# Optimization experiments

Measured on AMD Instinct MI355X. Metric: run time of the kernel, lower is better.

The kernel has to match this reference:

```python
import jax, jax.numpy as jnp
import numpy as np

N_STATE = 64
SEQ_L = 4096
BATCH, HCH = 16, 512
DT_MIN, DT_MAX = 0.001, 0.1


def _make_DPLR_HiPPO(N):
    # HiPPO-LegS matrix and its NPLR -> DPLR decomposition (annotated-s4).
    P = np.sqrt(1 + 2 * np.arange(N))
    A = P[:, None] * P[None, :]
    A = np.tril(A) - np.diag(np.arange(N))
    nhippo = -A
    p = 0.5 * np.sqrt(2 * np.arange(1, N + 1) + 1.0)
    q = 2 * p
    S = nhippo + p[:, None] * q[None, :]
    Lambda, V = np.linalg.eig(S)
    Vc = V.conj().T
    p_t = Vc @ p
    q_t = Vc @ q.conj()
    return Lambda, p_t, q_t, Vc


def _ri(z):
    return np.stack([z.real, z.imag], axis=-1).astype(np.float32)


def setup_inputs() -> dict:
    key = jax.random.key(0)
    k_u, k_ct, k_b, k_d, k_ls = jax.random.split(key, 5)
    Lambda, p, q, Vc = _make_DPLR_HiPPO(N_STATE)
    u = jax.random.normal(k_u, (BATCH, HCH, SEQ_L), dtype=jnp.float32)
    # lecun_normal params (fan_in = N)
    Ct_ri = jax.random.normal(k_ct, (1, N_STATE, 2), dtype=jnp.float32) / np.sqrt(N_STATE)
    Bp = jax.random.normal(k_b, (N_STATE, 1), dtype=jnp.float32) / np.sqrt(N_STATE)
    D = jax.random.uniform(k_d, (1,), dtype=jnp.float32)
    log_step = jax.random.uniform(
        k_ls, (1,), dtype=jnp.float32,
        minval=np.log(DT_MIN), maxval=np.log(DT_MAX))
    return {
        "u": u,
        "Lambda_ri": jnp.asarray(_ri(Lambda)),
        "p_ri": jnp.asarray(_ri(p)),
        "q_ri": jnp.asarray(_ri(q)),
        "Vc_ri": jnp.asarray(_ri(Vc)),
        "Ct_ri": Ct_ri,
        "Bp": Bp,
        "D": D,
        "log_step": log_step,
    }


def _cplx(x_ri):
    return x_ri[..., 0] + 1j * x_ri[..., 1]


def _s4_kernel(Lambda, p, q, B, Ct, step, L):
    # DPLR generating function evaluated at the L roots of unity (K_gen_DPLR
    # + conv_from_gen), vectorized over frequencies.
    Omega = jnp.exp((-2j * jnp.pi) * (jnp.arange(L) / L))          # (L,)
    g = (2.0 / step) * ((1.0 - Omega) / (1.0 + Omega))             # (L,)
    c = 2.0 / (1.0 + Omega)                                        # (L,)
    denom = g[:, None] - Lambda[None, :]                           # (L, N)
    cauchy = lambda v: (v[None, :] / denom).sum(-1)                # (L,)
    k00 = cauchy(Ct.conj() * B)
    k01 = cauchy(Ct.conj() * p)
    k10 = cauchy(q.conj() * B)
    k11 = cauchy(q.conj() * p)
    at_roots = c * (k00 - k01 * (1.0 / (1.0 + k11)) * k10)
    return jnp.fft.ifft(at_roots, L).real                          # (L,)


def reference(u, Lambda_ri, p_ri, q_ri, Vc_ri, Ct_ri, Bp, D, log_step):
    L = u.shape[-1]
    Lambda = _cplx(Lambda_ri)
    p = _cplx(p_ri)
    q = _cplx(q_ri)
    Vc = _cplx(Vc_ri)
    Ct = _cplx(Ct_ri).reshape(-1)                  # (N,)
    B = (Vc @ Bp.astype(Vc.dtype)).reshape(-1)     # (N,) complex
    step = jnp.exp(log_step)[0]
    K = _s4_kernel(Lambda, p, q, B, Ct, step, L).astype(u.dtype)   # (L,)
    # non-circular convolution via zero-padded FFT along the last axis
    n = 2 * L
    y = jnp.fft.irfft(jnp.fft.rfft(u, n=n) * jnp.fft.rfft(K, n=n), n=n)[..., :L]
    return y + D[0] * u
```

## Files before the change

kernel.cpp:

```cpp
#include <hip/hip_runtime.h>
#include <math.h>


#define SEQ_L 4096
#define M4    4096
#define NFFT  8192
#define NST   64
#define NROWS 8192
#define TWO_PI 6.28318530717958647692f

typedef float2 cf;

__device__ __forceinline__ cf cmul(cf a, cf b){ return make_float2(a.x*b.x - a.y*b.y, a.x*b.y + a.y*b.x); }
__device__ __forceinline__ cf cadd(cf a, cf b){ return make_float2(a.x+b.x, a.y+b.y); }
__device__ __forceinline__ cf csub(cf a, cf b){ return make_float2(a.x-b.x, a.y-b.y); }
__device__ __forceinline__ double2 dcmul(double2 a, double2 b) {
  return make_double2(a.x*b.x - a.y*b.y, a.x*b.y + a.y*b.x);
}

__device__ __forceinline__ int s2f(int i){ return i ^ (((i >> 6) & 1) << 3); }
__device__ __forceinline__ int s3f(int i){ return i ^ ((i >> 6) & 7) ^ (((i >> 6) & 1) << 3); }
__device__ __forceinline__ int smf(int i){ return i ^ ((i >> 6) & 7); }

template<int S>
__device__ __forceinline__ void r4(cf& a0, cf& a1, cf& a2, cf& a3){
  cf t0 = cadd(a0,a2), t1 = csub(a0,a2);
  cf t2 = cadd(a1,a3), t3 = csub(a1,a3);
  cf w = (S < 0) ? make_float2(t3.y, -t3.x) : make_float2(-t3.y, t3.x);
  a0 = cadd(t0,t2); a2 = csub(t0,t2);
  a1 = cadd(t1,w);  a3 = csub(t1,w);
}

template<int S, bool ZHI, bool LO4=false>
__device__ __forceinline__ void dft8(cf x[8]){
  const float C = 0.70710678118654752f;
  cf e0,e1,e2,e3,o0,o1,o2,o3;
  if (ZHI) {
    cf w  = (S<0)? make_float2(x[2].y,-x[2].x) : make_float2(-x[2].y,x[2].x);
    e0 = cadd(x[0],x[2]); e2 = csub(x[0],x[2]);
    e1 = cadd(x[0],w);    e3 = csub(x[0],w);
    cf w2 = (S<0)? make_float2(x[3].y,-x[3].x) : make_float2(-x[3].y,x[3].x);
    o0 = cadd(x[1],x[3]); o2 = csub(x[1],x[3]);
    o1 = cadd(x[1],w2);   o3 = csub(x[1],w2);
  } else {
    cf a0=x[0],a1=x[2],a2=x[4],a3=x[6];
    r4<S>(a0,a1,a2,a3);  e0=a0;e1=a1;e2=a2;e3=a3;
    cf b0=x[1],b1=x[3],b2=x[5],b3=x[7];
    r4<S>(b0,b1,b2,b3);  o0=b0;o1=b1;o2=b2;o3=b3;
  }
  x[0] = cadd(e0,o0); if (!LO4) x[4] = csub(e0,o0);
  cf t1 = (S<0)? make_float2(C*(o1.x+o1.y), C*(o1.y-o1.x))
               : make_float2(C*(o1.x-o1.y), C*(o1.x+o1.y));
  x[1] = cadd(e1,t1); if (!LO4) x[5] = csub(e1,t1);
  cf t2 = (S<0)? make_float2(o2.y,-o2.x) : make_float2(-o2.y,o2.x);
  x[2] = cadd(e2,t2); if (!LO4) x[6] = csub(e2,t2);
  cf t3 = (S<0)? make_float2(C*(o3.y-o3.x), -C*(o3.x+o3.y))
               : make_float2(-C*(o3.x+o3.y), C*(o3.x-o3.y));
  x[3] = cadd(e3,t3); if (!LO4) x[7] = csub(e3,t3);
}

__device__ __forceinline__ void chain8(cf x[8], float th){
  float sn, cs; __sincosf(th, &sn, &cs);
  cf w1 = make_float2(cs, sn);
  cf w2 = cmul(w1, w1);
  cf w3 = cmul(w2, w1);
  x[1] = cmul(x[1], w1); x[2] = cmul(x[2], w2); x[3] = cmul(x[3], w3);
  cf w4 = cmul(w2, w2);
  cf w5 = cmul(w3, w2);
  cf w6 = cmul(w3, w3);
  cf w7 = cmul(w4, w3);
  x[4] = cmul(x[4], w4); x[5] = cmul(x[5], w5); x[6] = cmul(x[6], w6);
  x[7] = cmul(x[7], w7);
}

__global__ __launch_bounds__(256) void k_at(
    const float* __restrict__ Lam_ri, const float* __restrict__ p_ri,
    const float* __restrict__ q_ri,  const float* __restrict__ Vc_ri,
    const float* __restrict__ Ct_ri, const float* __restrict__ Bp,
    const float* __restrict__ log_step, float2* __restrict__ atroots) {
  __shared__ double2 lam[NST], ctB[NST], ctp[NST], qB[NST], qp[NST];
  __shared__ double stepd;
  int tx = threadIdx.x;
  if (tx < NST) {
    int n = tx;
    double lr = Lam_ri[2*n], li = Lam_ri[2*n+1];
    double pr = p_ri[2*n],  pi = p_ri[2*n+1];
    double qr = q_ri[2*n],  qi = q_ri[2*n+1];
    double cr = Ct_ri[2*n], ci = Ct_ri[2*n+1];
    double br = 0.0, bi = 0.0;
    for (int m = 0; m < NST; ++m) {
      double b = (double)Bp[m];
      br += (double)Vc_ri[2*(n*NST+m)]   * b;
      bi += (double)Vc_ri[2*(n*NST+m)+1] * b;
    }
    lam[n] = make_double2(lr, li);
    ctB[n] = make_double2(cr*br + ci*bi, cr*bi - ci*br);
    ctp[n] = make_double2(cr*pr + ci*pi, cr*pi - ci*pr);
    qB[n]  = make_double2(qr*br + qi*bi, qr*bi - qi*br);
    qp[n]  = make_double2(qr*pr + qi*pi, qr*pi - qi*pr);
  }
  if (tx == 0) stepd = exp((double)log_step[0]);
  __syncthreads();
  int l = blockIdx.x * 256 + tx;
  double ang = -2.0 * M_PI * (double)l / (double)SEQ_L;
  double sn, cs;
  sincos(ang, &sn, &cs);
  double2 onem = make_double2(1.0 - cs, -sn);
  double2 onep = make_double2(1.0 + cs,  sn);
  double den = onep.x*onep.x + onep.y*onep.y;
  double2 ip = make_double2(onep.x/den, -onep.y/den);
  double2 g  = dcmul(onem, ip);
  double tw = 2.0 / stepd;
  g.x *= tw; g.y *= tw;
  double2 cc = make_double2(2.0*ip.x, 2.0*ip.y);
  double2 k00 = make_double2(0,0), k01 = make_double2(0,0);
  double2 k10 = make_double2(0,0), k11 = make_double2(0,0);
  for (int n = 0; n < NST; ++n) {
    double2 L = lam[n];
    double2 d = make_double2(g.x - L.x, g.y - L.y);
    double dd = d.x*d.x + d.y*d.y;
    double2 inv = make_double2(d.x/dd, -d.y/dd);
    double2 v;
    v = ctB[n]; k00.x += v.x*inv.x - v.y*inv.y; k00.y += v.x*inv.y + v.y*inv.x;
    v = ctp[n]; k01.x += v.x*inv.x - v.y*inv.y; k01.y += v.x*inv.y + v.y*inv.x;
    v = qB[n];  k10.x += v.x*inv.x - v.y*inv.y; k10.y += v.x*inv.y + v.y*inv.x;
    v = qp[n];  k11.x += v.x*inv.x - v.y*inv.y; k11.y += v.x*inv.y + v.y*inv.x;
  }
  double2 k11p = make_double2(1.0 + k11.x, k11.y);
  double2 num  = dcmul(k01, k10);
  double dd2 = k11p.x*k11p.x + k11p.y*k11p.y;
  double2 t = make_double2((num.x*k11p.x + num.y*k11p.y)/dd2,
                           (num.y*k11p.x - num.x*k11p.y)/dd2);
  double2 inner = make_double2(k00.x - t.x, k00.y - t.y);
  double2 at = dcmul(cc, inner);
  atroots[l] = make_float2((float)at.x, (float)at.y);
}

__global__ __launch_bounds__(512) void k_kt(const float2* __restrict__ atroots,
                                            float* __restrict__ Kt) {
  int gid  = blockIdx.x * 512 + threadIdx.x;
  int t    = gid >> 6;
  int lane = gid & 63;
  float acc = 0.f;
  for (int l = lane; l < SEQ_L; l += 64) {
    int ph = (l * t) & (SEQ_L - 1);
    float a = (float)ph * (TWO_PI / (float)SEQ_L);
    float sn, cs; __sincosf(a, &sn, &cs);
    float2 v = atroots[l];
    acc += v.x*cs - v.y*sn;
  }
  for (int off = 32; off > 0; off >>= 1) acc += __shfl_down(acc, off, 64);
  if (lane == 0) Kt[t] = acc * (1.0f / (float)SEQ_L);
}

__global__ __launch_bounds__(256) void k_geven(const float2* __restrict__ atroots,
                                               float2* __restrict__ G) {
  int l = blockIdx.x * 256 + threadIdx.x;
  if (l > 2048) return;
  float2 a = atroots[l];
  float2 b = atroots[(M4 - l) & (M4 - 1)];
  G[2*l] = make_float2(0.5f*(a.x + b.x), 0.5f*(a.y - b.y));
}

__global__ __launch_bounds__(512) void k_godd(const float* __restrict__ Kt,
                                              float2* __restrict__ G) {
  int gid  = blockIdx.x * 512 + threadIdx.x;
  int w    = gid >> 6;
  int k    = 2*w + 1;
  int lane = gid & 63;
  float ar = 0.f, ai = 0.f;
  for (int t = lane; t < SEQ_L; t += 64) {
    int ph = (k * t) & (NFFT - 1);
    float a = (float)ph * (-TWO_PI / (float)NFFT);
    float sn, cs; __sincosf(a, &sn, &cs);
    float kv = Kt[t];
    ar += kv * cs; ai += kv * sn;
  }
  for (int off = 32; off > 0; off >>= 1) {
    ar += __shfl_down(ar, off, 64);
    ai += __shfl_down(ai, off, 64);
  }
  if (lane == 0) G[k] = make_float2(ar, ai);
}

__global__ __launch_bounds__(256) void k_ab(const float2* __restrict__ G,
                                            float4* __restrict__ ab) {
  int idx = blockIdx.x * 256 + threadIdx.x;
  int tidc = idx >> 3, d = idx & 7;
  int k = (tidc >> 6) + 8*((tidc >> 3) & 7) + 64*(tidc & 7) + 512*d;
  double ang = -2.0 * M_PI * (double)k / (double)NFFT;
  double sn, cs; sincos(ang, &sn, &cs);
  double2 a = make_double2(0.5*(1.0 + sn), -0.5*cs);
  double2 b = make_double2(0.5*(1.0 - sn),  0.5*cs);
  double2 p = make_double2(0.5*(1.0 + sn),  0.5*cs);
  double2 q = make_double2(0.5*(1.0 - sn), -0.5*cs);
  float2 gk = G[k];
  float2 gh = G[M4 - k];
  double2 Gk = make_double2(gk.x, gk.y);
  double2 Gh = make_double2(gh.x, -gh.y);
  double2 pa = dcmul(p, a), pb = dcmul(p, b);
  double2 qa = dcmul(q, a), qb = dcmul(q, b);
  double2 al = dcmul(pa, Gk), t1 = dcmul(qb, Gh);
  al.x += t1.x; al.y += t1.y;
  double2 be = dcmul(pb, Gk), t2 = dcmul(qa, Gh);
  be.x += t2.x; be.y += t2.y;
  const double s = 1.0 / (double)M4;
  ab[idx] = make_float4((float)(al.x*s), (float)(al.y*s),
                        (float)(be.x*s), (float)(be.y*s));
}

__global__ __launch_bounds__(512) void k_conv(const float* __restrict__ u,
                                              const float4* __restrict__ ab,
                                              const float* __restrict__ Dp,
                                              float* __restrict__ out) {
  __shared__ cf lds[M4];
  const int tid = threadIdx.x;
  const size_t row = blockIdx.x;
  const float2* ru = (const float2*)(u + row * SEQ_L);
  const int a1 = tid >> 6, t0 = tid & 63, b2 = (tid >> 3) & 7, t00 = tid & 7;

  cf x[8];
  #pragma unroll
  for (int m = 0; m < 4; ++m) { float2 v = ru[tid + 512*m]; x[m] = make_float2(v.x, v.y); }
  #pragma unroll
  for (int m = 4; m < 8; ++m) x[m] = make_float2(0.f, 0.f);

  dft8<-1, true>(x);
  chain8(x, -TWO_PI * (float)tid / (float)M4);
  #pragma unroll
  for (int a = 0; a < 8; ++a) lds[a*512 + tid] = x[a];
  __syncthreads();
  #pragma unroll
  for (int r = 0; r < 8; ++r) x[r] = lds[a1*512 + t0 + 64*r];
  dft8<-1, false>(x);
  chain8(x, -TWO_PI * (float)t0 / 512.f);
  __syncthreads();
  #pragma unroll
  for (int b = 0; b < 8; ++b) lds[s2f(a1*512 + b*64 + t0)] = x[b];
  __syncthreads();
  #pragma unroll
  for (int r = 0; r < 8; ++r) x[r] = lds[s2f(a1*512 + b2*64 + t00 + 8*r)];
  dft8<-1, false>(x);
  chain8(x, -TWO_PI * (float)t00 / 64.f);
  __syncthreads();
  #pragma unroll
  for (int c = 0; c < 8; ++c) lds[s3f(a1*512 + b2*64 + c*8 + t00)] = x[c];
  __syncthreads();
  #pragma unroll
  for (int r = 0; r < 8; ++r) x[r] = lds[s3f(a1*512 + b2*64 + t00*8 + r)];
  dft8<-1, false>(x);
  __syncthreads();

  const int base = a1 + 8*b2 + 64*t00;
  #pragma unroll
  for (int d = 0; d < 8; ++d) lds[smf(base + 512*d)] = x[d];
  __syncthreads();
  const float4* abp = ab + (size_t)tid * 8;
  #pragma unroll
  for (int d = 0; d < 8; ++d) {
    cf t = lds[smf((M4 - base - 512*d) & (M4 - 1))];
    float4 c = abp[d];
    x[d] = make_float2(c.x*x[d].x - c.y*x[d].y + c.z*t.x + c.w*t.y,
                       c.x*x[d].y + c.y*x[d].x + c.w*t.x - c.z*t.y);
  }
  __syncthreads();

  dft8<1, false>(x);
  #pragma unroll
  for (int r = 0; r < 8; ++r) lds[s3f(a1*512 + b2*64 + t00*8 + r)] = x[r];
  __syncthreads();
  #pragma unroll
  for (int c = 0; c < 8; ++c) x[c] = lds[s3f(a1*512 + b2*64 + c*8 + t00)];
  chain8(x, TWO_PI * (float)t00 / 64.f);
  dft8<1, false>(x);
  __syncthreads();
  #pragma unroll
  for (int r = 0; r < 8; ++r) lds[s2f(a1*512 + b2*64 + t00 + 8*r)] = x[r];
  __syncthreads();
  #pragma unroll
  for (int b = 0; b < 8; ++b) x[b] = lds[s2f(a1*512 + b*64 + t0)];
  chain8(x, TWO_PI * (float)t0 / 512.f);
  dft8<1, false>(x);
  __syncthreads();
  #pragma unroll
  for (int r = 0; r < 8; ++r) lds[a1*512 + t0 + 64*r] = x[r];
  __syncthreads();
  #pragma unroll
  for (int a = 0; a < 8; ++a) x[a] = lds[a*512 + tid];
  chain8(x, TWO_PI * (float)tid / (float)M4);
  dft8<1, false, true>(x);

  const float Dv = Dp[0];
  float2* o = (float2*)(out + row * SEQ_L);
  #pragma unroll
  for (int m = 0; m < 4; ++m) {
    float2 uv = ru[tid + 512*m];
    o[tid + 512*m] = make_float2(x[m].x + Dv*uv.x, x[m].y + Dv*uv.y);
  }
}

extern "C" void kernel_launch(void* const* d_in, const int* in_sizes, int n_in,
                              void* d_out, int out_size, void* d_ws, size_t ws_size,
                              hipStream_t stream) {
  const float* u      = (const float*)d_in[0];
  const float* Lam_ri = (const float*)d_in[1];
  const float* p_ri   = (const float*)d_in[2];
  const float* q_ri   = (const float*)d_in[3];
  const float* Vc_ri  = (const float*)d_in[4];
  const float* Ct_ri  = (const float*)d_in[5];
  const float* Bp     = (const float*)d_in[6];
  const float* Dp     = (const float*)d_in[7];
  const float* ls     = (const float*)d_in[8];

  char* ws = (char*)d_ws;
  float2* atroots = (float2*)(ws);
  float*  Kt      = (float*) (ws + 32768);
  float2* G       = (float2*)(ws + 49152);
  float4* ab      = (float4*)(ws + 81936);

  k_at   <<<dim3(SEQ_L/256), dim3(256), 0, stream>>>(Lam_ri, p_ri, q_ri, Vc_ri, Ct_ri, Bp, ls, atroots);
  k_kt   <<<dim3(512),  dim3(512), 0, stream>>>(atroots, Kt);
  k_geven<<<dim3(9),    dim3(256), 0, stream>>>(atroots, G);
  k_godd <<<dim3(256),  dim3(512), 0, stream>>>(Kt, G);
  k_ab   <<<dim3(16),   dim3(256), 0, stream>>>(G, ab);
  k_conv <<<dim3(NROWS), dim3(512), 0, stream>>>(u, ab, Dp, (float*)d_out);
}
```

Baseline: 209.3 us.

## Replace direct-DFT kernel spectrum with single-block 8192-point radix-8 FFT

Drops the k_geven and k_godd kernels, which built the zero-padded spectrum of K from an O(N^2) direct DFT with sincos per term. A new single-workgroup k_G kernel instead runs an 8192-point FFT in LDS using radix-8 stages, a 16-point twiddle and a final radix-2 butterfly done with lane shuffles. This removes a launch and a large amount of trig arithmetic. The trade is that the work now runs on a single 1024-thread block, and the even bins now come from the FFT rather than from atroots.

Result: faster. 198.6 us (-5.1%).

```diff
diff --git a/kernel.cpp b/kernel.cpp
--- a/kernel.cpp
+++ b/kernel.cpp
@@ -21,6 +21,7 @@
 __device__ __forceinline__ int s2f(int i){ return i ^ (((i >> 6) & 1) << 3); }
 __device__ __forceinline__ int s3f(int i){ return i ^ ((i >> 6) & 7) ^ (((i >> 6) & 1) << 3); }
 __device__ __forceinline__ int smf(int i){ return i ^ ((i >> 6) & 7); }
+__device__ __forceinline__ int sw(int p){ return p ^ ((p >> 4) & 15); }
 
 template<int S>
 __device__ __forceinline__ void r4(cf& a0, cf& a1, cf& a2, cf& a3){
@@ -71,6 +72,40 @@
   cf w7 = cmul(w4, w3);
   x[4] = cmul(x[4], w4); x[5] = cmul(x[5], w5); x[6] = cmul(x[6], w6);
   x[7] = cmul(x[7], w7);
+}
+
+__device__ __forceinline__ constexpr float c16t(int d){
+  return (d==1)?0.92387953251128675613f:(d==2)?0.70710678118654752440f:
+         (d==3)?0.38268343236508977173f:(d==4)?0.f:
+         (d==5)?-0.38268343236508977173f:(d==6)?-0.70710678118654752440f:
+         -0.92387953251128675613f;
+}
+__device__ __forceinline__ constexpr float s16t(int d){
+  return (d==1)?0.38268343236508977173f:(d==2)?0.70710678118654752440f:
+         (d==3)?0.92387953251128675613f:(d==4)?1.f:
+         (d==5)?0.92387953251128675613f:(d==6)?0.70710678118654752440f:
+         0.38268343236508977173f;
+}
+template<int S>
+__device__ __forceinline__ void tw16(cf x[8], int t000){
+  #pragma unroll
+  for (int d = 1; d < 8; ++d) {
+    float ce = t000 ? c16t(d) : 1.f;
+    float se = t000 ? ((S < 0) ? -s16t(d) : s16t(d)) : 0.f;
+    cf a = x[d];
+    x[d] = make_float2(a.x*ce - a.y*se, a.x*se + a.y*ce);
+  }
+}
+
+__device__ __forceinline__ void r2_shfl(cf x[8], int tid){
+  const float sgn = (tid & 1) ? -1.f : 1.f;
+  #pragma unroll
+  for (int k = 0; k < 8; ++k) {
+    float ox = __shfl_xor(x[k].x, 1, 64);
+    float oy = __shfl_xor(x[k].y, 1, 64);
+    x[k].x = ox + sgn * x[k].x;
+    x[k].y = oy + sgn * x[k].y;
+  }
 }
 
 __global__ __launch_bounds__(256) void k_at(
@@ -153,34 +188,48 @@
   if (lane == 0) Kt[t] = acc * (1.0f / (float)SEQ_L);
 }
 
-__global__ __launch_bounds__(256) void k_geven(const float2* __restrict__ atroots,
-                                               float2* __restrict__ G) {
-  int l = blockIdx.x * 256 + threadIdx.x;
-  if (l > 2048) return;
-  float2 a = atroots[l];
-  float2 b = atroots[(M4 - l) & (M4 - 1)];
-  G[2*l] = make_float2(0.5f*(a.x + b.x), 0.5f*(a.y - b.y));
-}
-
-__global__ __launch_bounds__(512) void k_godd(const float* __restrict__ Kt,
-                                              float2* __restrict__ G) {
-  int gid  = blockIdx.x * 512 + threadIdx.x;
-  int w    = gid >> 6;
-  int k    = 2*w + 1;
-  int lane = gid & 63;
-  float ar = 0.f, ai = 0.f;
-  for (int t = lane; t < SEQ_L; t += 64) {
-    int ph = (k * t) & (NFFT - 1);
-    float a = (float)ph * (-TWO_PI / (float)NFFT);
-    float sn, cs; __sincosf(a, &sn, &cs);
-    float kv = Kt[t];
-    ar += kv * cs; ai += kv * sn;
-  }
-  for (int off = 32; off > 0; off >>= 1) {
-    ar += __shfl_down(ar, off, 64);
-    ai += __shfl_down(ai, off, 64);
-  }
-  if (lane == 0) G[k] = make_float2(ar, ai);
+__global__ __launch_bounds__(1024) void k_G(const float* __restrict__ Kt,
+                                            float2* __restrict__ G) {
+  __shared__ cf lds[NFFT];
+  int tid = threadIdx.x;
+  cf x[8];
+  #pragma unroll
+  for (int m = 0; m < 4; ++m) x[m] = make_float2(Kt[tid + 1024*m], 0.f);
+  #pragma unroll
+  for (int m = 4; m < 8; ++m) x[m] = make_float2(0.f, 0.f);
+  const int a1 = tid >> 7, t0 = tid & 127, b2 = (tid >> 4) & 7, t00 = tid & 15;
+  const int c3 = (tid >> 1) & 7, t000 = tid & 1;
+  dft8<-1, true>(x);
+  chain8(x, -TWO_PI * (float)tid / (float)NFFT);
+  #pragma unroll
+  for (int a = 0; a < 8; ++a) lds[sw(a*1024 + tid)] = x[a];
+  __syncthreads();
+  #pragma unroll
+  for (int r = 0; r < 8; ++r) x[r] = lds[sw(a1*1024 + t0 + 128*r)];
+  dft8<-1, false>(x);
+  chain8(x, -TWO_PI * (float)t0 / 1024.f);
+  __syncthreads();
+  #pragma unroll
+  for (int b = 0; b < 8; ++b) lds[sw(a1*1024 + b*128 + t0)] = x[b];
+  __syncthreads();
+  #pragma unroll
+  for (int r = 0; r < 8; ++r) x[r] = lds[sw(a1*1024 + b2*128 + t00 + 16*r)];
+  dft8<-1, false>(x);
+  chain8(x, -TWO_PI * (float)t00 / 128.f);
+  __syncthreads();
+  #pragma unroll
+  for (int c = 0; c < 8; ++c) lds[sw(a1*1024 + b2*128 + c*16 + t00)] = x[c];
+  __syncthreads();
+  #pragma unroll
+  for (int r = 0; r < 8; ++r) x[r] = lds[sw(a1*1024 + b2*128 + c3*16 + t000 + 2*r)];
+  dft8<-1, false>(x);
+  tw16<-1>(x, t000);
+  r2_shfl(x, tid);
+  #pragma unroll
+  for (int d = 0; d < 8; ++d) {
+    int bin = a1 + 8*b2 + 64*c3 + 512*d + 4096*t000;
+    if (bin <= M4) G[bin] = x[d];
+  }
 }
 
 __global__ __launch_bounds__(256) void k_ab(const float2* __restrict__ G,
@@ -318,10 +367,9 @@
   float2* G       = (float2*)(ws + 49152);
   float4* ab      = (float4*)(ws + 81936);
 
-  k_at   <<<dim3(SEQ_L/256), dim3(256), 0, stream>>>(Lam_ri, p_ri, q_ri, Vc_ri, Ct_ri, Bp, ls, atroots);
-  k_kt   <<<dim3(512),  dim3(512), 0, stream>>>(atroots, Kt);
-  k_geven<<<dim3(9),    dim3(256), 0, stream>>>(atroots, G);
-  k_godd <<<dim3(256),  dim3(512), 0, stream>>>(Kt, G);
-  k_ab   <<<dim3(16),   dim3(256), 0, stream>>>(G, ab);
-  k_conv <<<dim3(NROWS), dim3(512), 0, stream>>>(u, ab, Dp, (float*)d_out);
-}
+  k_at  <<<dim3(SEQ_L/256), dim3(256), 0, stream>>>(Lam_ri, p_ri, q_ri, Vc_ri, Ct_ri, Bp, ls, atroots);
+  k_kt  <<<dim3(512),  dim3(512), 0, stream>>>(atroots, Kt);
+  k_G   <<<dim3(1),    dim3(1024), 0, stream>>>(Kt, G);
+  k_ab  <<<dim3(16),   dim3(256), 0, stream>>>(G, ab);
+  k_conv<<<dim3(NROWS), dim3(512), 0, stream>>>(u, ab, Dp, (float*)d_out);
+}
```
